# Kernel optimization log

Hardware: AMD Instinct MI355X
Metric: run time of the kernel (lower is better)

Reference implementation:

```python
import jax, jax.numpy as jnp
import numpy as np

FRAME, LATENT, HIDDEN, GATE_H, EXPERTS = 267, 32, 256, 64, 6
BATCH = 4096
IN0 = LATENT + FRAME            # 299: decoder layer-0 input (z, c)
IN1 = LATENT + HIDDEN           # 288: decoder layer-1/2 input (z, h)
OUT = FRAME                     # num_future_predictions * frame_size


def _lin(key, fan_in, fan_out):
    b = np.sqrt(1.0 / fan_in)
    return jax.random.uniform(key, (fan_in, fan_out), jnp.float32, -b, b)


def setup_inputs() -> dict:
    key = jax.random.key(0)
    ks = jax.random.split(key, 16)
    d = {
        "x": jax.random.normal(ks[0], (BATCH, FRAME), jnp.float32),
        "c": jax.random.normal(ks[1], (BATCH, FRAME), jnp.float32),
        "eps": jax.random.normal(ks[2], (BATCH, LATENT), jnp.float32),
        # encoder
        "enc_w1": _lin(ks[3], 2 * FRAME, HIDDEN), "enc_b1": jnp.zeros((HIDDEN,), jnp.float32),
        "enc_w2": _lin(ks[4], FRAME + HIDDEN, HIDDEN), "enc_b2": jnp.zeros((HIDDEN,), jnp.float32),
        "enc_wmu": _lin(ks[5], FRAME + HIDDEN, LATENT), "enc_bmu": jnp.zeros((LATENT,), jnp.float32),
        "enc_wlv": _lin(ks[6], FRAME + HIDDEN, LATENT), "enc_blv": jnp.zeros((LATENT,), jnp.float32),
        # gate MLP
        "g_w0": _lin(ks[7], IN0, GATE_H), "g_b0": jnp.zeros((GATE_H,), jnp.float32),
        "g_w1": _lin(ks[8], GATE_H, GATE_H), "g_b1": jnp.zeros((GATE_H,), jnp.float32),
        "g_w2": _lin(ks[9], GATE_H, EXPERTS), "g_b2": jnp.zeros((EXPERTS,), jnp.float32),
        # expert-mixed decoder layers (kaiming-uniform-ish init, bias 0.01)
        "w0": jax.random.uniform(ks[10], (EXPERTS, IN0, HIDDEN), jnp.float32, -np.sqrt(6.0 / IN0), np.sqrt(6.0 / IN0)),
        "b0": jnp.full((EXPERTS, HIDDEN), 0.01, jnp.float32),
        "w1": jax.random.uniform(ks[11], (EXPERTS, IN1, HIDDEN), jnp.float32, -np.sqrt(6.0 / IN1), np.sqrt(6.0 / IN1)),
        "b1": jnp.full((EXPERTS, HIDDEN), 0.01, jnp.float32),
        "w2": jax.random.uniform(ks[12], (EXPERTS, IN1, OUT), jnp.float32, -np.sqrt(6.0 / IN1), np.sqrt(6.0 / IN1)),
        "b2": jnp.full((EXPERTS, OUT), 0.01, jnp.float32),
    }
    return d


def reference(x, c, eps,
              enc_w1, enc_b1, enc_w2, enc_b2, enc_wmu, enc_bmu, enc_wlv, enc_blv,
              g_w0, g_b0, g_w1, g_b1, g_w2, g_b2,
              w0, b0, w1, b1, w2, b2):
    elu = jax.nn.elu
    # --- encoder ---
    h1 = elu(jnp.concatenate([x, c], axis=1) @ enc_w1 + enc_b1)
    h2 = elu(jnp.concatenate([x, h1], axis=1) @ enc_w2 + enc_b2)
    s = jnp.concatenate([x, h2], axis=1)
    mu = s @ enc_wmu + enc_bmu
    logvar = s @ enc_wlv + enc_blv
    z = mu + eps * jnp.exp(0.5 * logvar)
    # --- gate ---
    zc = jnp.concatenate([z, c], axis=1)
    g = elu(zc @ g_w0 + g_b0)
    g = elu(g @ g_w1 + g_b1)
    coeff = jax.nn.softmax(g @ g_w2 + g_b2, axis=1)  # [N, E]
    # --- soft-MoE decoder: blended-weight per-sample GEMMs ---
    layer = c
    for w, b, act in ((w0, b0, elu), (w1, b1, elu), (w2, b2, None)):
        inp = jnp.concatenate([z, layer], axis=1)  # [N, Din]
        # out[n,o] = sum_e coeff[n,e] * (inp[n,:] @ w[e,:,o]) + coeff[n,:] @ b[:,o]
        out = jnp.einsum('ne,ni,eio->no', coeff, inp, w) + coeff @ b
        layer = act(out) if act is not None else out
    return layer, mu, logvar
```

## Files before the change

kernel.cpp:

```cpp
#include <hip/hip_runtime.h>
#include <hip/hip_bf16.h>
#include <math.h>

#define N_BATCH 4096
#define FRAME   267
#define LATENT  32
#define HIDDEN  256
#define GATE_H  64
#define EXPERTS 6

typedef __hip_bfloat16 bf16;
typedef __bf16  bf16x8 __attribute__((ext_vector_type(8)));
typedef float   f32x4  __attribute__((ext_vector_type(4)));

__device__ __forceinline__ float eluf(float v) { return (v > 0.f) ? v : (expf(v) - 1.f); }

#define MFMA(a, b, p) __builtin_amdgcn_mfma_f32_16x16x32_bf16((a), (b), (p), 0, 0, 0)

struct WEnt { const float* src; bf16* dst; int K, M, Mtot, mOff, Ksteps, Mtiles, cum; };
struct WTab { WEnt e[10]; int total; };

__global__ __launch_bounds__(256) void prep_kernel(
    const float* __restrict__ bmu, const float* __restrict__ blv,
    float* __restrict__ biasCat, WTab tab)
{
    const int tid = threadIdx.x, bid = blockIdx.x;
    if (bid == 0 && tid < 64)
        biasCat[tid] = (tid < 32) ? bmu[tid] : blv[tid - 32];

    __shared__ float tbuf[32][33];
    int i = 0;
    while (i < 9 && bid >= tab.e[i + 1].cum) ++i;
    const WEnt en = tab.e[i];
    const int t = bid - en.cum;
    const int perE = en.Ksteps * en.Mtiles;
    const int e = t / perE;
    const int rr = t - e * perE;
    const int mt = rr / en.Ksteps;
    const int ks = rr - mt * en.Ksteps;
    const int tx = tid & 31, ty = tid >> 5;
    const float* src = en.src + (size_t)e * en.K * en.M;
    #pragma unroll
    for (int i0 = 0; i0 < 32; i0 += 8) {
        const int k = ks * 32 + i0 + ty, m = mt * 32 + tx;
        tbuf[i0 + ty][tx] = (k < en.K && m < en.M) ? src[(size_t)k * en.M + m] : 0.f;
    }
    __syncthreads();
    bf16* dst = en.dst + ((size_t)(e * en.Ksteps + ks) * en.Mtot + en.mOff + mt * 32) * 32;
    #pragma unroll
    for (int i0 = 0; i0 < 32; i0 += 8)
        dst[(size_t)(i0 + ty) * 32 + tx] = __float2bfloat16(tbuf[tx][i0 + ty]);
}

__global__ __launch_bounds__(1024, 4) void fused_kernel(
    const float* __restrict__ x, const float* __restrict__ c,
    const float* __restrict__ eps,
    const bf16* __restrict__ We1, const float* __restrict__ eb1,
    const bf16* __restrict__ We2, const float* __restrict__ eb2,
    const bf16* __restrict__ Wml, const float* __restrict__ biasCat,
    const bf16* __restrict__ Wg0, const float* __restrict__ gb0,
    const bf16* __restrict__ Wg1, const float* __restrict__ gb1,
    const bf16* __restrict__ Wg2, const float* __restrict__ gb2,
    const bf16* __restrict__ W0, const float* __restrict__ b0,
    const bf16* __restrict__ W1, const float* __restrict__ b1,
    const bf16* __restrict__ W2, const float* __restrict__ b2,
    float* __restrict__ out_layer, float* __restrict__ out_mu,
    float* __restrict__ out_lv)
{
    __shared__ bf16  bufA[16 * 552];
    __shared__ bf16  bufB[16 * 552];
    __shared__ float sMLp[4][16 * 64];
    __shared__ bf16  sG1[16 * 72];
    __shared__ bf16  sG2[16 * 72];
    __shared__ float sLg[16 * 16];
    __shared__ float sCo[EXPERTS * 16];

    const int tid  = threadIdx.x;
    const int w    = tid >> 6, lane = tid & 63, ml = lane & 15, quad = lane >> 4;
    const int row0 = blockIdx.x * 16;

    {
        const float* xr = x + (size_t)(row0 + w) * FRAME;
        const float* cr = c + (size_t)(row0 + w) * FRAME;
        #pragma unroll
        for (int j = 0; j < 9; ++j) {
            const int col = lane + j * 64;
            if (col < 544) {
                float v = 0.f;
                if (col < FRAME)          v = xr[col];
                else if (col < 2 * FRAME) v = cr[col - FRAME];
                bufA[w * 552 + col] = __float2bfloat16(v);
            }
        }
    }
    __syncthreads();

    {
        const int col = 16 * w + ml;
        const bf16* wq = We1 + (size_t)col * 32 + quad * 8;
        f32x4 acc = (f32x4){0,0,0,0};
        bf16x8 bb[8];
        #pragma unroll
        for (int j = 0; j < 8; ++j) bb[j] = *(const bf16x8*)(wq + (size_t)j * 8192);
        #pragma unroll
        for (int u = 0; u < 17; ++u) {
            const bf16x8 b = bb[u & 7];
            if (u + 8 < 17) bb[u & 7] = *(const bf16x8*)(wq + (size_t)(u + 8) * 8192);
            acc = MFMA(*(const bf16x8*)(bufA + ml * 552 + u * 32 + quad * 8), b, acc);
        }
        const float bv = eb1[col];
        #pragma unroll
        for (int rg = 0; rg < 4; ++rg)
            bufB[(quad * 4 + rg) * 552 + 267 + col] = __float2bfloat16(eluf(acc[rg] + bv));
        #pragma unroll
        for (int j = 0; j < 5; ++j) {
            const int cc = lane + j * 64;
            if (cc < 267) bufB[w * 552 + cc] = bufA[w * 552 + cc];
        }
        if (lane < 21) bufB[w * 552 + 523 + lane] = __float2bfloat16(0.f);
    }
    __syncthreads();

    {
        const int col = 16 * w + ml;
        const bf16* wq = We2 + (size_t)col * 32 + quad * 8;
        f32x4 acc = (f32x4){0,0,0,0};
        bf16x8 bb[8];
        #pragma unroll
        for (int j = 0; j < 8; ++j) bb[j] = *(const bf16x8*)(wq + (size_t)j * 8192);
        #pragma unroll
        for (int u = 0; u < 17; ++u) {
            const bf16x8 b = bb[u & 7];
            if (u + 8 < 17) bb[u & 7] = *(const bf16x8*)(wq + (size_t)(u + 8) * 8192);
            acc = MFMA(*(const bf16x8*)(bufB + ml * 552 + u * 32 + quad * 8), b, acc);
        }
        __syncthreads();
        const float bv = eb2[col];
        #pragma unroll
        for (int rg = 0; rg < 4; ++rg)
            bufB[(quad * 4 + rg) * 552 + 267 + col] = __float2bfloat16(eluf(acc[rg] + bv));
    }
    __syncthreads();

    {
        const int t = w & 3, kg = w >> 2;
        const int col = 16 * t + ml;
        const int k0 = kg * 4, k1 = (kg == 3) ? 17 : kg * 4 + 4;
        const bf16* wq = Wml + (size_t)col * 32 + quad * 8;
        f32x4 p = (f32x4){0,0,0,0};
        #pragma unroll
        for (int u = 0; u < 5; ++u) {
            const int ks = k0 + u;
            if (ks < k1)
                p = MFMA(*(const bf16x8*)(bufB + ml * 552 + ks * 32 + quad * 8),
                         *(const bf16x8*)(wq + (size_t)ks * 2048), p);
        }
        #pragma unroll
        for (int rg = 0; rg < 4; ++rg)
            sMLp[kg][(quad * 4 + rg) * 64 + col] = p[rg];
    }
    __syncthreads();

    if (tid < 512) {
        const int r = tid >> 5, l = tid & 31;
        const float m  = sMLp[0][r * 64 + l] + sMLp[1][r * 64 + l]
                       + sMLp[2][r * 64 + l] + sMLp[3][r * 64 + l] + biasCat[l];
        const float lv = sMLp[0][r * 64 + 32 + l] + sMLp[1][r * 64 + 32 + l]
                       + sMLp[2][r * 64 + 32 + l] + sMLp[3][r * 64 + 32 + l] + biasCat[32 + l];
        const int gi = (row0 + r) * LATENT + l;
        out_mu[gi] = m; out_lv[gi] = lv;
        const bf16 zb = __float2bfloat16(m + eps[gi] * expf(0.5f * lv));
        bufA[r * 552 + l] = zb;
        bufB[r * 552 + l] = zb;
        #pragma unroll
        for (int j = 0; j < 9; ++j) {
            const int col = 32 + l + j * 32;
            bf16 v = __float2bfloat16(0.f);
            if (col < 299) v = bufA[r * 552 + 267 + (col - 32)];
            bufB[r * 552 + col] = v;
        }
    }
    __syncthreads();

    {
        const int col = 16 * w + ml;
        const bf16* wq = W0 + (size_t)col * 32 + quad * 8;
        f32x4 pe[6] = {(f32x4){0,0,0,0}, (f32x4){0,0,0,0}, (f32x4){0,0,0,0},
                       (f32x4){0,0,0,0}, (f32x4){0,0,0,0}, (f32x4){0,0,0,0}};

        if (w < 4) {
            const int gc = 16 * w + ml;
            const bf16* gq = Wg0 + (size_t)gc * 32 + quad * 8;
            f32x4 p = (f32x4){0,0,0,0};
            #pragma unroll
            for (int ks = 0; ks < 10; ++ks)
                p = MFMA(*(const bf16x8*)(bufB + ml * 552 + ks * 32 + quad * 8),
                         *(const bf16x8*)(gq + (size_t)ks * 2048), p);
            const float bv = gb0[gc];
            #pragma unroll
            for (int rg = 0; rg < 4; ++rg)
                sG1[(quad * 4 + rg) * 72 + gc] = __float2bfloat16(eluf(p[rg] + bv));
        }
        {
            bf16x8 bb[8];
            #pragma unroll
            for (int j = 0; j < 8; ++j) bb[j] = *(const bf16x8*)(wq + (size_t)j * 8192);
            #pragma unroll
            for (int v = 0; v < 30; ++v) {
                const bf16x8 b = bb[v & 7];
                if (v + 8 < 30) bb[v & 7] = *(const bf16x8*)(wq + (size_t)(v + 8) * 8192);
                pe[v / 10] = MFMA(*(const bf16x8*)(bufB + ml * 552 + (v % 10) * 32 + quad * 8),
                                  b, pe[v / 10]);
            }
        }
        __syncthreads();

        if (w == 0) {
            #pragma unroll
            for (int t = 0; t < 4; ++t) {
                const int gc = 16 * t + ml;
                const bf16* gq = Wg1 + (size_t)gc * 32 + quad * 8;
                f32x4 p = (f32x4){0,0,0,0};
                #pragma unroll
                for (int ks = 0; ks < 2; ++ks)
                    p = MFMA(*(const bf16x8*)(sG1 + ml * 72 + ks * 32 + quad * 8),
                             *(const bf16x8*)(gq + (size_t)ks * 2048), p);
                const float bv = gb1[gc];
                #pragma unroll
                for (int rg = 0; rg < 4; ++rg)
                    sG2[(quad * 4 + rg) * 72 + gc] = __float2bfloat16(eluf(p[rg] + bv));
            }
            {
                const bf16* gq = Wg2 + (size_t)ml * 32 + quad * 8;
                f32x4 p = (f32x4){0,0,0,0};
                #pragma unroll
                for (int ks = 0; ks < 2; ++ks)
                    p = MFMA(*(const bf16x8*)(sG2 + ml * 72 + ks * 32 + quad * 8),
                             *(const bf16x8*)(gq + (size_t)ks * 1024), p);
                const float bv = (ml < EXPERTS) ? gb2[ml] : 0.f;
                #pragma unroll
                for (int rg = 0; rg < 4; ++rg)
                    sLg[(quad * 4 + rg) * 16 + ml] = p[rg] + bv;
            }
            if (lane < 16) {
                float v[EXPERTS];
                float m = -1e30f;
                #pragma unroll
                for (int i = 0; i < EXPERTS; ++i) { v[i] = sLg[lane * 16 + i]; m = fmaxf(m, v[i]); }
                float s = 0.f;
                #pragma unroll
                for (int i = 0; i < EXPERTS; ++i) { v[i] = expf(v[i] - m); s += v[i]; }
                const float inv = 1.f / s;
                #pragma unroll
                for (int i = 0; i < EXPERTS; ++i) sCo[i * 16 + lane] = v[i] * inv;
            }
        }
        {
            bf16x8 bb[8];
            #pragma unroll
            for (int j = 0; j < 8; ++j) bb[j] = *(const bf16x8*)(wq + (size_t)(30 + j) * 8192);
            #pragma unroll
            for (int v = 0; v < 30; ++v) {
                const bf16x8 b = bb[v & 7];
                if (v + 8 < 30) bb[v & 7] = *(const bf16x8*)(wq + (size_t)(30 + v + 8) * 8192);
                const int u = 30 + v;
                pe[u / 10] = MFMA(*(const bf16x8*)(bufB + ml * 552 + (u % 10) * 32 + quad * 8),
                                  b, pe[u / 10]);
            }
        }
        __syncthreads();

        f32x4 acc = (f32x4){0,0,0,0};
        #pragma unroll
        for (int e = 0; e < EXPERTS; ++e) {
            const float bv = b0[e * 256 + col];
            #pragma unroll
            for (int rg = 0; rg < 4; ++rg)
                acc[rg] += sCo[e * 16 + quad * 4 + rg] * (pe[e][rg] + bv);
        }
        #pragma unroll
        for (int rg = 0; rg < 4; ++rg)
            bufA[(quad * 4 + rg) * 552 + 32 + col] = __float2bfloat16(eluf(acc[rg]));
    }
    __syncthreads();

    {
        const int col = 16 * w + ml;
        const bf16* wq = W1 + (size_t)col * 32 + quad * 8;
        f32x4 pe[6] = {(f32x4){0,0,0,0}, (f32x4){0,0,0,0}, (f32x4){0,0,0,0},
                       (f32x4){0,0,0,0}, (f32x4){0,0,0,0}, (f32x4){0,0,0,0}};
        bf16x8 bb[8];
        #pragma unroll
        for (int j = 0; j < 8; ++j) bb[j] = *(const bf16x8*)(wq + (size_t)j * 8192);
        #pragma unroll
        for (int u = 0; u < 54; ++u) {
            const bf16x8 b = bb[u & 7];
            if (u + 8 < 54) bb[u & 7] = *(const bf16x8*)(wq + (size_t)(u + 8) * 8192);
            pe[u / 9] = MFMA(*(const bf16x8*)(bufA + ml * 552 + (u % 9) * 32 + quad * 8),
                             b, pe[u / 9]);
        }
        f32x4 acc = (f32x4){0,0,0,0};
        #pragma unroll
        for (int e = 0; e < EXPERTS; ++e) {
            const float bv = b1[e * 256 + col];
            #pragma unroll
            for (int rg = 0; rg < 4; ++rg)
                acc[rg] += sCo[e * 16 + quad * 4 + rg] * (pe[e][rg] + bv);
        }
        #pragma unroll
        for (int rg = 0; rg < 4; ++rg)
            bufB[(quad * 4 + rg) * 552 + 32 + col] = __float2bfloat16(eluf(acc[rg]));
    }
    __syncthreads();

    {
        for (int t = w; t < 17; t += 16) {
            const int col = 16 * t + ml;
            const bf16* wq = W2 + (size_t)col * 32 + quad * 8;
            f32x4 pe[6] = {(f32x4){0,0,0,0}, (f32x4){0,0,0,0}, (f32x4){0,0,0,0},
                           (f32x4){0,0,0,0}, (f32x4){0,0,0,0}, (f32x4){0,0,0,0}};
            bf16x8 bb[8];
            #pragma unroll
            for (int j = 0; j < 8; ++j) bb[j] = *(const bf16x8*)(wq + (size_t)j * 10240);
            #pragma unroll
            for (int u = 0; u < 54; ++u) {
                const bf16x8 b = bb[u & 7];
                if (u + 8 < 54) bb[u & 7] = *(const bf16x8*)(wq + (size_t)(u + 8) * 10240);
                pe[u / 9] = MFMA(*(const bf16x8*)(bufB + ml * 552 + (u % 9) * 32 + quad * 8),
                                 b, pe[u / 9]);
            }
            f32x4 acc = (f32x4){0,0,0,0};
            #pragma unroll
            for (int e = 0; e < EXPERTS; ++e) {
                const float bv = (col < FRAME) ? b2[e * FRAME + col] : 0.f;
                #pragma unroll
                for (int rg = 0; rg < 4; ++rg)
                    acc[rg] += sCo[e * 16 + quad * 4 + rg] * (pe[e][rg] + bv);
            }
            if (col < FRAME) {
                #pragma unroll
                for (int rg = 0; rg < 4; ++rg)
                    out_layer[(size_t)(row0 + quad * 4 + rg) * FRAME + col] = acc[rg];
            }
        }
    }
}

extern "C" void kernel_launch(void* const* d_in, const int* in_sizes, int n_in,
                              void* d_out, int out_size, void* d_ws, size_t ws_size,
                              hipStream_t stream) {
    const float* x       = (const float*)d_in[0];
    const float* c       = (const float*)d_in[1];
    const float* eps     = (const float*)d_in[2];
    const float* enc_w1  = (const float*)d_in[3];
    const float* enc_b1  = (const float*)d_in[4];
    const float* enc_w2  = (const float*)d_in[5];
    const float* enc_b2  = (const float*)d_in[6];
    const float* enc_wmu = (const float*)d_in[7];
    const float* enc_bmu = (const float*)d_in[8];
    const float* enc_wlv = (const float*)d_in[9];
    const float* enc_blv = (const float*)d_in[10];
    const float* g_w0    = (const float*)d_in[11];
    const float* g_b0    = (const float*)d_in[12];
    const float* g_w1    = (const float*)d_in[13];
    const float* g_b1    = (const float*)d_in[14];
    const float* g_w2    = (const float*)d_in[15];
    const float* g_b2    = (const float*)d_in[16];
    const float* w0      = (const float*)d_in[17];
    const float* b0      = (const float*)d_in[18];
    const float* w1      = (const float*)d_in[19];
    const float* b1      = (const float*)d_in[20];
    const float* w2      = (const float*)d_in[21];
    const float* b2      = (const float*)d_in[22];

    float* out_layer = (float*)d_out;
    float* out_mu    = out_layer + (size_t)N_BATCH * FRAME;
    float* out_lv    = out_mu    + (size_t)N_BATCH * LATENT;

    char* p = (char*)d_ws;
    float* biasCat = (float*)p;  p += 64 * 4;
    bf16* Wt_e1 = (bf16*)p;      p += (size_t)17 * 256 * 32 * 2;
    bf16* Wt_e2 = (bf16*)p;      p += (size_t)17 * 256 * 32 * 2;
    bf16* Wt_ml = (bf16*)p;      p += (size_t)17 * 64 * 32 * 2;
    bf16* Wt_g0 = (bf16*)p;      p += (size_t)10 * 64 * 32 * 2;
    bf16* Wt_g1 = (bf16*)p;      p += (size_t)2 * 64 * 32 * 2;
    bf16* Wt_g2 = (bf16*)p;      p += (size_t)2 * 32 * 32 * 2;
    bf16* Wt_w0 = (bf16*)p;      p += (size_t)EXPERTS * 10 * 256 * 32 * 2;
    bf16* Wt_w1 = (bf16*)p;      p += (size_t)EXPERTS * 9 * 256 * 32 * 2;
    bf16* Wt_w2 = (bf16*)p;      p += (size_t)EXPERTS * 9 * 320 * 32 * 2;

    WTab tab;
    int cum = 0, n = 0;
    auto add = [&](const float* src, bf16* dst, int K, int M, int Mtot, int mOff, int E) {
        int Ksteps;
        if (K == 534 || K == 523) Ksteps = 17;
        else if (K == 299) Ksteps = 10;
        else if (K == 288) Ksteps = 9;
        else Ksteps = 2;
        const int Mtiles = (M + 31) / 32;
        tab.e[n] = {src, dst, K, M, Mtot, mOff, Ksteps, Mtiles, cum};
        cum += E * Ksteps * Mtiles;
        ++n;
    };
    add(enc_w1,  Wt_e1, 534, 256, 256, 0, 1);
    add(enc_w2,  Wt_e2, 523, 256, 256, 0, 1);
    add(enc_wmu, Wt_ml, 523, 32, 64, 0, 1);
    add(enc_wlv, Wt_ml, 523, 32, 64, 32, 1);
    add(g_w0,    Wt_g0, 299, 64, 64, 0, 1);
    add(g_w1,    Wt_g1, 64, 64, 64, 0, 1);
    add(g_w2,    Wt_g2, 64, 6, 32, 0, 1);
    add(w0,      Wt_w0, 299, 256, 256, 0, EXPERTS);
    add(w1,      Wt_w1, 288, 256, 256, 0, EXPERTS);
    add(w2,      Wt_w2, 288, 267, 320, 0, EXPERTS);
    tab.total = cum;

    prep_kernel<<<dim3(cum), dim3(256), 0, stream>>>(enc_bmu, enc_blv, biasCat, tab);

    fused_kernel<<<dim3(N_BATCH / 16), dim3(1024), 0, stream>>>(
        x, c, eps,
        Wt_e1, enc_b1, Wt_e2, enc_b2, Wt_ml, biasCat,
        Wt_g0, g_b0, Wt_g1, g_b1, Wt_g2, g_b2,
        Wt_w0, b0, Wt_w1, b1, Wt_w2, b2,
        out_layer, out_mu, out_lv);
}
```

Measured before the change: 166.9 us.

## Stream weight tiles through LDS via global_load_lds instead of register prefetch

Replaces the 8-deep register prefetch ring of B-operand weight fragments in every GEMM stage with direct global-to-LDS loads (global_load_lds) into a per-wave 4 KB staging area. Each group of four k-steps is loaded, drained with s_waitcnt vmcnt(0), then consumed from LDS. This removes the register pressure of holding eight prefetched fragments, which may allow better occupancy. In exchange, the full drain before each group serializes load latency with the MFMAs instead of overlapping it, and 64 KB of extra shared memory is added.

```diff
diff --git a/kernel.cpp b/kernel.cpp
--- a/kernel.cpp
+++ b/kernel.cpp
@@ -16,6 +16,14 @@
 __device__ __forceinline__ float eluf(float v) { return (v > 0.f) ? v : (expf(v) - 1.f); }
 
 #define MFMA(a, b, p) __builtin_amdgcn_mfma_f32_16x16x32_bf16((a), (b), (p), 0, 0, 0)
+#define VMDRAIN() asm volatile("s_waitcnt vmcnt(0)" ::: "memory")
+#define CFENCE()  asm volatile("" ::: "memory")
+
+__device__ __forceinline__ void gload16(const bf16* g, char* l) {
+    __builtin_amdgcn_global_load_lds(
+        (const __attribute__((address_space(1))) void*)g,
+        (__attribute__((address_space(3))) void*)l, 16, 0, 0);
+}
 
 struct WEnt { const float* src; bf16* dst; int K, M, Mtot, mOff, Ksteps, Mtiles, cum; };
 struct WTab { WEnt e[10]; int total; };
@@ -74,10 +82,12 @@
     __shared__ bf16  sG2[16 * 72];
     __shared__ float sLg[16 * 16];
     __shared__ float sCo[EXPERTS * 16];
+    __shared__ char  sStg[16 * 4096];
 
     const int tid  = threadIdx.x;
     const int w    = tid >> 6, lane = tid & 63, ml = lane & 15, quad = lane >> 4;
     const int row0 = blockIdx.x * 16;
+    char* stg = sStg + w * 4096;
 
     {
         const float* xr = x + (size_t)(row0 + w) * FRAME;
@@ -99,14 +109,18 @@
         const int col = 16 * w + ml;
         const bf16* wq = We1 + (size_t)col * 32 + quad * 8;
         f32x4 acc = (f32x4){0,0,0,0};
-        bf16x8 bb[8];
-        #pragma unroll
-        for (int j = 0; j < 8; ++j) bb[j] = *(const bf16x8*)(wq + (size_t)j * 8192);
-        #pragma unroll
-        for (int u = 0; u < 17; ++u) {
-            const bf16x8 b = bb[u & 7];
-            if (u + 8 < 17) bb[u & 7] = *(const bf16x8*)(wq + (size_t)(u + 8) * 8192);
-            acc = MFMA(*(const bf16x8*)(bufA + ml * 552 + u * 32 + quad * 8), b, acc);
+        #pragma unroll
+        for (int cc = 0; cc < 17; cc += 4) {
+            #pragma unroll
+            for (int j = 0; j < 4; ++j)
+                if (cc + j < 17) gload16(wq + (size_t)(cc + j) * 8192, stg + j * 1024);
+            VMDRAIN();
+            #pragma unroll
+            for (int j = 0; j < 4; ++j)
+                if (cc + j < 17)
+                    acc = MFMA(*(const bf16x8*)(bufA + ml * 552 + (cc + j) * 32 + quad * 8),
+                               *(const bf16x8*)(stg + j * 1024 + lane * 16), acc);
+            CFENCE();
         }
         const float bv = eb1[col];
         #pragma unroll
@@ -125,14 +139,18 @@
         const int col = 16 * w + ml;
         const bf16* wq = We2 + (size_t)col * 32 + quad * 8;
         f32x4 acc = (f32x4){0,0,0,0};
-        bf16x8 bb[8];
-        #pragma unroll
-        for (int j = 0; j < 8; ++j) bb[j] = *(const bf16x8*)(wq + (size_t)j * 8192);
-        #pragma unroll
-        for (int u = 0; u < 17; ++u) {
-            const bf16x8 b = bb[u & 7];
-            if (u + 8 < 17) bb[u & 7] = *(const bf16x8*)(wq + (size_t)(u + 8) * 8192);
-            acc = MFMA(*(const bf16x8*)(bufB + ml * 552 + u * 32 + quad * 8), b, acc);
+        #pragma unroll
+        for (int cc = 0; cc < 17; cc += 4) {
+            #pragma unroll
+            for (int j = 0; j < 4; ++j)
+                if (cc + j < 17) gload16(wq + (size_t)(cc + j) * 8192, stg + j * 1024);
+            VMDRAIN();
+            #pragma unroll
+            for (int j = 0; j < 4; ++j)
+                if (cc + j < 17)
+                    acc = MFMA(*(const bf16x8*)(bufB + ml * 552 + (cc + j) * 32 + quad * 8),
+                               *(const bf16x8*)(stg + j * 1024 + lane * 16), acc);
+            CFENCE();
         }
         __syncthreads();
         const float bv = eb2[col];
@@ -201,17 +219,20 @@
             for (int rg = 0; rg < 4; ++rg)
                 sG1[(quad * 4 + rg) * 72 + gc] = __float2bfloat16(eluf(p[rg] + bv));
         }
-        {
-            bf16x8 bb[8];
-            #pragma unroll
-            for (int j = 0; j < 8; ++j) bb[j] = *(const bf16x8*)(wq + (size_t)j * 8192);
-            #pragma unroll
-            for (int v = 0; v < 30; ++v) {
-                const bf16x8 b = bb[v & 7];
-                if (v + 8 < 30) bb[v & 7] = *(const bf16x8*)(wq + (size_t)(v + 8) * 8192);
-                pe[v / 10] = MFMA(*(const bf16x8*)(bufB + ml * 552 + (v % 10) * 32 + quad * 8),
-                                  b, pe[v / 10]);
-            }
+        #pragma unroll
+        for (int cc = 0; cc < 30; cc += 4) {
+            #pragma unroll
+            for (int j = 0; j < 4; ++j)
+                if (cc + j < 30) gload16(wq + (size_t)(cc + j) * 8192, stg + j * 1024);
+            VMDRAIN();
+            #pragma unroll
+            for (int j = 0; j < 4; ++j)
+                if (cc + j < 30) {
+                    const int u = cc + j;
+                    pe[u / 10] = MFMA(*(const bf16x8*)(bufB + ml * 552 + (u % 10) * 32 + quad * 8),
+                                      *(const bf16x8*)(stg + j * 1024 + lane * 16), pe[u / 10]);
+                }
+            CFENCE();
         }
         __syncthreads();
 
@@ -255,18 +276,20 @@
                 for (int i = 0; i < EXPERTS; ++i) sCo[i * 16 + lane] = v[i] * inv;
             }
         }
-        {
-            bf16x8 bb[8];
-            #pragma unroll
-            for (int j = 0; j < 8; ++j) bb[j] = *(const bf16x8*)(wq + (size_t)(30 + j) * 8192);
-            #pragma unroll
-            for (int v = 0; v < 30; ++v) {
-                const bf16x8 b = bb[v & 7];
-                if (v + 8 < 30) bb[v & 7] = *(const bf16x8*)(wq + (size_t)(30 + v + 8) * 8192);
-                const int u = 30 + v;
-                pe[u / 10] = MFMA(*(const bf16x8*)(bufB + ml * 552 + (u % 10) * 32 + quad * 8),
-                                  b, pe[u / 10]);
-            }
+        #pragma unroll
+        for (int cc = 30; cc < 60; cc += 4) {
+            #pragma unroll
+            for (int j = 0; j < 4; ++j)
+                if (cc + j < 60) gload16(wq + (size_t)(cc + j) * 8192, stg + j * 1024);
+            VMDRAIN();
+            #pragma unroll
+            for (int j = 0; j < 4; ++j)
+                if (cc + j < 60) {
+                    const int u = cc + j;
+                    pe[u / 10] = MFMA(*(const bf16x8*)(bufB + ml * 552 + (u % 10) * 32 + quad * 8),
+                                      *(const bf16x8*)(stg + j * 1024 + lane * 16), pe[u / 10]);
+                }
+            CFENCE();
         }
         __syncthreads();
 
@@ -289,15 +312,20 @@
         const bf16* wq = W1 + (size_t)col * 32 + quad * 8;
         f32x4 pe[6] = {(f32x4){0,0,0,0}, (f32x4){0,0,0,0}, (f32x4){0,0,0,0},
                        (f32x4){0,0,0,0}, (f32x4){0,0,0,0}, (f32x4){0,0,0,0}};
-        bf16x8 bb[8];
-        #pragma unroll
-        for (int j = 0; j < 8; ++j) bb[j] = *(const bf16x8*)(wq + (size_t)j * 8192);
-        #pragma unroll
-        for (int u = 0; u < 54; ++u) {
-            const bf16x8 b = bb[u & 7];
-            if (u + 8 < 54) bb[u & 7] = *(const bf16x8*)(wq + (size_t)(u + 8) * 8192);
-            pe[u / 9] = MFMA(*(const bf16x8*)(bufA + ml * 552 + (u % 9) * 32 + quad * 8),
-                             b, pe[u / 9]);
+        #pragma unroll
+        for (int cc = 0; cc < 54; cc += 4) {
+            #pragma unroll
+            for (int j = 0; j < 4; ++j)
+                if (cc + j < 54) gload16(wq + (size_t)(cc + j) * 8192, stg + j * 1024);
+            VMDRAIN();
+            #pragma unroll
+            for (int j = 0; j < 4; ++j)
+                if (cc + j < 54) {
+                    const int u = cc + j;
+                    pe[u / 9] = MFMA(*(const bf16x8*)(bufA + ml * 552 + (u % 9) * 32 + quad * 8),
+                                     *(const bf16x8*)(stg + j * 1024 + lane * 16), pe[u / 9]);
+                }
+            CFENCE();
         }
         f32x4 acc = (f32x4){0,0,0,0};
         #pragma unroll
@@ -319,15 +347,20 @@
             const bf16* wq = W2 + (size_t)col * 32 + quad * 8;
             f32x4 pe[6] = {(f32x4){0,0,0,0}, (f32x4){0,0,0,0}, (f32x4){0,0,0,0},
                            (f32x4){0,0,0,0}, (f32x4){0,0,0,0}, (f32x4){0,0,0,0}};
-            bf16x8 bb[8];
-            #pragma unroll
-            for (int j = 0; j < 8; ++j) bb[j] = *(const bf16x8*)(wq + (size_t)j * 10240);
-            #pragma unroll
-            for (int u = 0; u < 54; ++u) {
-                const bf16x8 b = bb[u & 7];
-                if (u + 8 < 54) bb[u & 7] = *(const bf16x8*)(wq + (size_t)(u + 8) * 10240);
-                pe[u / 9] = MFMA(*(const bf16x8*)(bufB + ml * 552 + (u % 9) * 32 + quad * 8),
-                                 b, pe[u / 9]);
+            #pragma unroll
+            for (int cc = 0; cc < 54; cc += 4) {
+                #pragma unroll
+                for (int j = 0; j < 4; ++j)
+                    if (cc + j < 54) gload16(wq + (size_t)(cc + j) * 10240, stg + j * 1024);
+                VMDRAIN();
+                #pragma unroll
+                for (int j = 0; j < 4; ++j)
+                    if (cc + j < 54) {
+                        const int u = cc + j;
+                        pe[u / 9] = MFMA(*(const bf16x8*)(bufB + ml * 552 + (u % 9) * 32 + quad * 8),
+                                         *(const bf16x8*)(stg + j * 1024 + lane * 16), pe[u / 9]);
+                    }
+                CFENCE();
             }
             f32x4 acc = (f32x4){0,0,0,0};
             #pragma unroll
```

After: 173.4 us. 3.9% more time.
